# Kernel optimization log

Hardware: AMD Instinct MI355X
Metric: run time of the kernel (lower is better)

The kernel has to match this reference:

```python
import jax, jax.numpy as jnp
import numpy as np

D_MODEL = 512; D_INNER = 1024; D_STATE = 16; DT_RANK = 32; D_CONV = 4
N_LAYERS = 2; LSPP = 7; N_ROI = 2048; HIDDEN = 4096


def layer_norm(x, g, b, eps=1e-5):
    mu = x.mean(-1, keepdims=True)
    v = ((x - mu) ** 2).mean(-1, keepdims=True)
    return (x - mu) * jax.lax.rsqrt(v + eps) * g + b


def causal_dwconv(u, w, b):
    # u: [N,L,Di], w: [Di,K] depthwise, causal left-pad K-1
    x = jnp.transpose(u, (0, 2, 1))
    out = jax.lax.conv_general_dilated(x, w[:, None, :], (1,), [(D_CONV - 1, 0)],
                                       dimension_numbers=('NCH', 'OIH', 'NCH'),
                                       feature_group_count=D_INNER)
    return jnp.transpose(out, (0, 2, 1)) + b


def selective_scan(u, dt, A, B, C):
    # u, dt: [N,L,Di]; B, C: [N,L,S]; A: [Di,S]
    def step(h, xs):
        dt_t, B_t, C_t, u_t = xs
        dA = jnp.exp(dt_t[..., None] * A)                      # [N,Di,S]
        h = dA * h + (dt_t * u_t)[..., None] * B_t[:, None, :]
        return h, jnp.einsum('nds,ns->nd', h, C_t)
    h0 = jnp.zeros((u.shape[0], D_INNER, D_STATE), u.dtype)
    xs = (jnp.moveaxis(dt, 1, 0), jnp.moveaxis(B, 1, 0),
          jnp.moveaxis(C, 1, 0), jnp.moveaxis(u, 1, 0))
    _, ys = jax.lax.scan(step, h0, xs)
    return jnp.moveaxis(ys, 0, 1)                              # [N,L,Di]


def mamba_block(h, inw, cw, cb, xpw, dtw, dtb, Alog, Dp, ow):
    # decomposed bidirectional mamba ('dbm'): shared in_proj/gate, fwd+bwd scans summed
    xz = h @ inw.T                                             # [N,L,2*Di]
    xi, z = jnp.split(xz, 2, axis=-1)
    ys = []
    for d in range(2):
        u = xi if d == 0 else jnp.flip(xi, axis=1)
        u = jax.nn.silu(causal_dwconv(u, cw[d], cb[d]))
        dbl = u @ xpw[d].T                                     # [N,L,DT_RANK+2S]
        dtr = dbl[..., :DT_RANK]
        B = dbl[..., DT_RANK:DT_RANK + D_STATE]
        C = dbl[..., DT_RANK + D_STATE:]
        dt = jax.nn.softplus(dtr @ dtw[d].T + dtb[d])
        A = -jnp.exp(Alog[d])
        yd = selective_scan(u, dt, A, B, C) + u * Dp[d]
        ys.append(yd if d == 0 else jnp.flip(yd, axis=1))
    return ((ys[0] + ys[1]) * jax.nn.silu(z)) @ ow.T


def setup_inputs() -> dict:
    key = jax.random.key(0)
    ks = iter(jax.random.split(key, 40))
    rn = lambda shape, scale: jax.random.normal(next(ks), shape, dtype=jnp.float32) * scale
    inp = {}
    inp['x_flat'] = rn((N_ROI, D_MODEL * LSPP), 1.0)
    inp['conv_a_w'] = rn((256, 512, 3), (512 * 3) ** -0.5)
    inp['conv_p_w'] = rn((256, 512, 1), 512 ** -0.5)
    inp['se_w1'] = rn((32, 512), 512 ** -0.5)
    inp['se_b1'] = jnp.zeros((32,), jnp.float32)
    inp['se_w2'] = rn((512, 32), 32 ** -0.5)
    inp['se_b2'] = jnp.zeros((512,), jnp.float32)
    inp['ln_g'] = jnp.ones((N_LAYERS, D_MODEL), jnp.float32)
    inp['ln_b'] = jnp.zeros((N_LAYERS, D_MODEL), jnp.float32)
    inp['in_proj_w'] = rn((N_LAYERS, 2 * D_INNER, D_MODEL), D_MODEL ** -0.5)
    inp['conv_w'] = rn((N_LAYERS, 2, D_INNER, D_CONV), D_CONV ** -0.5)
    inp['conv_b'] = jnp.zeros((N_LAYERS, 2, D_INNER), jnp.float32)
    inp['x_proj_w'] = rn((N_LAYERS, 2, DT_RANK + 2 * D_STATE, D_INNER), D_INNER ** -0.5)
    inp['dt_proj_w'] = rn((N_LAYERS, 2, D_INNER, DT_RANK), DT_RANK ** -0.5)
    inp['dt_proj_b'] = rn((N_LAYERS, 2, D_INNER), 0.1) - 4.0
    inp['A_log'] = jnp.log(jnp.arange(1., D_STATE + 1., dtype=jnp.float32)) * jnp.ones((N_LAYERS, 2, D_INNER, D_STATE), jnp.float32)
    inp['D_param'] = jnp.ones((N_LAYERS, 2, D_INNER), jnp.float32)
    inp['out_proj_w'] = rn((N_LAYERS, D_MODEL, D_INNER), D_INNER ** -0.5)
    inp['out_ln_g'] = jnp.ones((D_MODEL,), jnp.float32)
    inp['out_ln_b'] = jnp.zeros((D_MODEL,), jnp.float32)
    inp['mlp_w1'] = rn((HIDDEN, D_MODEL), D_MODEL ** -0.5)
    inp['mlp_b1'] = jnp.zeros((HIDDEN,), jnp.float32)
    inp['mlp_w2'] = rn((HIDDEN, HIDDEN), HIDDEN ** -0.5)
    inp['mlp_b2'] = jnp.zeros((HIDDEN,), jnp.float32)
    return inp


def reference(x_flat, conv_a_w, conv_p_w, se_w1, se_b1, se_w2, se_b2, ln_g, ln_b,
              in_proj_w, conv_w, conv_b, x_proj_w, dt_proj_w, dt_proj_b, A_log,
              D_param, out_proj_w, out_ln_g, out_ln_b, mlp_w1, mlp_b1, mlp_w2, mlp_b2):
    N = x_flat.shape[0]
    x = x_flat.reshape(N, D_MODEL, LSPP)                       # [N,512,7]
    dn = ('NCH', 'OIH', 'NCH')
    # TSSE: strided conv branch + maxpool branch, concat, SE gating; L: 7 -> 4
    a = jax.nn.relu(jax.lax.conv_general_dilated(x, conv_a_w, (2,), [(1, 1)], dimension_numbers=dn))
    p = jax.lax.reduce_window(x, -jnp.inf, jax.lax.max, (1, 1, 3), (1, 1, 2), ((0, 0), (0, 0), (1, 1)))
    p = jax.nn.relu(jax.lax.conv_general_dilated(p, conv_p_w, (1,), [(0, 0)], dimension_numbers=dn))
    y = jnp.concatenate([a, p], axis=1)                        # [N,512,4]
    s = jax.nn.sigmoid(jax.nn.relu(y.mean(-1) @ se_w1.T + se_b1) @ se_w2.T + se_b2)
    y = y * s[:, :, None]
    # Mamba backbone: 2 pre-norm residual DBM blocks (mask is all-ones -> no-op)
    h = jnp.transpose(y, (0, 2, 1))                            # [N,L,512]
    for l in range(N_LAYERS):
        h = h + mamba_block(layer_norm(h, ln_g[l], ln_b[l]), in_proj_w[l], conv_w[l],
                            conv_b[l], x_proj_w[l], dt_proj_w[l], dt_proj_b[l],
                            A_log[l], D_param[l], out_proj_w[l])
    h = layer_norm(h, out_ln_g, out_ln_b)
    feat = h.mean(1)                                           # mean pool over time
    z1 = jax.nn.relu(feat @ mlp_w1.T + mlp_b1)
    return jax.nn.relu(z1 @ mlp_w2.T + mlp_b2)                 # [N,4096]
```

## Files before the change

kernel.cpp:

```cpp
#include <hip/hip_runtime.h>
#include <hip/hip_bf16.h>

typedef __hip_bfloat16 bf16;
typedef __attribute__((ext_vector_type(8))) short s16x8;
typedef __attribute__((ext_vector_type(4))) float f32x4;

__device__ __forceinline__ float u2f(unsigned short u){
  union { unsigned int i; float f; } v; v.i = ((unsigned int)u) << 16; return v.f;
}
__device__ __forceinline__ float bfu(bf16 x){ return __bfloat162float(x); }
__device__ __forceinline__ bf16  f2b(float x){ return __float2bfloat16(x); }

__device__ __forceinline__ void gload16(const void* g, void* l){
  __builtin_amdgcn_global_load_lds(
      (const __attribute__((address_space(1))) void*)g,
      (__attribute__((address_space(3))) void*)l, 16, 0, 0);
}

__device__ __forceinline__ float block_sum256(float v, float* red){
  #pragma unroll
  for (int o = 32; o > 0; o >>= 1) v += __shfl_down(v, o, 64);
  int lane = threadIdx.x & 63, wid = threadIdx.x >> 6;
  if (lane == 0) red[wid] = v;
  __syncthreads();
  float r = red[0] + red[1] + red[2] + red[3];
  __syncthreads();
  return r;
}

__global__ __launch_bounds__(256) void f2b4_kernel(
    const float4* __restrict__ in, ushort4* __restrict__ out, int n4)
{
  int stride = gridDim.x * 256;
  for (int i = blockIdx.x*256 + threadIdx.x; i < n4; i += stride){
    float4 v = in[i];
    ushort4 o;
    o.x = __bfloat16_as_ushort(f2b(v.x));
    o.y = __bfloat16_as_ushort(f2b(v.y));
    o.z = __bfloat16_as_ushort(f2b(v.z));
    o.w = __bfloat16_as_ushort(f2b(v.w));
    out[i] = o;
  }
}

__global__ __launch_bounds__(256) void xpw_pad_kernel(
    const float* __restrict__ xpw, bf16* __restrict__ out)
{
  int idx = blockIdx.x*256 + threadIdx.x;
  if (idx >= 524288) return;
  int l = idx >> 18, rem = idx & 262143, row = rem >> 10, c = rem & 1023;
  int d = row >> 7, r = row & 127;
  float v = (r < 64) ? xpw[(((size_t)l*2 + d)*64 + r)*1024 + c] : 0.f;
  out[idx] = f2b(v);
}

template<int ACT, int OMODE, bool HASBIAS>
__global__ __launch_bounds__(256) void mgemm_kernel(
    const bf16* __restrict__ A, const bf16* __restrict__ W,
    const float* __restrict__ bias, void* __restrict__ outp,
    int K, int ldo)
{
  __shared__ char lsA[16384];
  __shared__ char lsB[16384];
  const int tid = threadIdx.x;
  const int w = tid >> 6, l = tid & 63;
  const int nwg = gridDim.x * gridDim.y;
  const int lin = blockIdx.y * gridDim.x + blockIdx.x;
  const int cpx = nwg >> 3;
  const int swz = (lin & 7) * cpx + (lin >> 3);
  const int m0 = (swz % gridDim.x) * 128, n0 = (swz / gridDim.x) * 128;
  const int wr = w >> 1, wc = w & 1;
  const size_t ldb = (size_t)K * 2;
  const char* Ab = (const char*)A + (size_t)m0 * ldb;
  const char* Wb = (const char*)W + (size_t)n0 * ldb;

  const int srow = l >> 3;
  const int scb  = ((l & 7) ^ srow) << 4;

  const int fr = l & 15;
  const int fg = l >> 4;
  const int fsw = (fr & 7) << 4;

  f32x4 acc[4][4];
  #pragma unroll
  for (int m = 0; m < 4; ++m)
    #pragma unroll
    for (int n = 0; n < 4; ++n) acc[m][n] = (f32x4){0.f,0.f,0.f,0.f};

  const int nk = K >> 6;
  for (int kt = 0; kt < nk; ++kt){
    const char* As = Ab + (size_t)kt * 128;
    const char* Ws = Wb + (size_t)kt * 128;
    #pragma unroll
    for (int i = 0; i < 4; ++i){
      int row = (i*4 + w)*8 + srow;
      gload16(As + (size_t)row*ldb + scb, &lsA[(i*4 + w)*1024]);
    }
    #pragma unroll
    for (int i = 0; i < 4; ++i){
      int row = (i*4 + w)*8 + srow;
      gload16(Ws + (size_t)row*ldb + scb, &lsB[(i*4 + w)*1024]);
    }
    __syncthreads();

    s16x8 af[4][2], bfr[4][2];
    #pragma unroll
    for (int m = 0; m < 4; ++m){
      int row = wr*64 + m*16 + fr;
      af[m][0] = *(const s16x8*)&lsA[row*128 + (( 0 + fg*16) ^ fsw)];
      af[m][1] = *(const s16x8*)&lsA[row*128 + ((64 + fg*16) ^ fsw)];
    }
    #pragma unroll
    for (int n = 0; n < 4; ++n){
      int row = wc*64 + n*16 + fr;
      bfr[n][0] = *(const s16x8*)&lsB[row*128 + (( 0 + fg*16) ^ fsw)];
      bfr[n][1] = *(const s16x8*)&lsB[row*128 + ((64 + fg*16) ^ fsw)];
    }
    #pragma unroll
    for (int m = 0; m < 4; ++m)
      #pragma unroll
      for (int n = 0; n < 4; ++n){
        acc[m][n] = __builtin_amdgcn_mfma_f32_16x16x32_bf16(af[m][0], bfr[n][0], acc[m][n], 0, 0, 0);
        acc[m][n] = __builtin_amdgcn_mfma_f32_16x16x32_bf16(af[m][1], bfr[n][1], acc[m][n], 0, 0, 0);
      }
    __syncthreads();
  }

  const int orow0 = m0 + wr*64, ocol0 = n0 + wc*64;
  #pragma unroll
  for (int n = 0; n < 4; ++n){
    int col = ocol0 + n*16 + fr;
    float bv = HASBIAS ? bias[col] : 0.f;
    #pragma unroll
    for (int m = 0; m < 4; ++m){
      int rbase = orow0 + m*16 + fg*4;
      #pragma unroll
      for (int r = 0; r < 4; ++r){
        float v = acc[m][n][r] + bv;
        if (ACT == 1) v = fmaxf(v, 0.f);
        size_t oi = (size_t)(rbase + r) * ldo + col;
        if (OMODE == 0)      ((bf16*)outp)[oi] = f2b(v);
        else if (OMODE == 1) ((float*)outp)[oi] = v;
        else                 ((float*)outp)[oi] += v;
      }
    }
  }
}

__global__ __launch_bounds__(256) void bgemm_kernel(
    const bf16* __restrict__ A, const bf16* __restrict__ W,
    float* __restrict__ outp)
{
  __shared__ char lsA[16384];
  __shared__ char lsB[16384];
  const int tid = threadIdx.x;
  const int w = tid >> 6, l = tid & 63;
  const int nwg = gridDim.x * 2;
  const int lin = blockIdx.y * gridDim.x + blockIdx.x;
  const int cpx = nwg >> 3;
  const int swz = (lin & 7) * cpx + (lin >> 3);
  const int m0 = (swz % gridDim.x) * 128;
  const int d  = swz / gridDim.x;
  const int K = 1024, ldo = 256;
  const int wr = w >> 1, wc = w & 1;
  const size_t ldb = (size_t)K * 2;
  const char* Ab = (const char*)(A + (size_t)d*8388608) + (size_t)m0 * ldb;
  const char* Wb = (const char*)(W + (size_t)d*131072);

  const int srow = l >> 3;
  const int scb  = ((l & 7) ^ srow) << 4;
  const int fr = l & 15;
  const int fg = l >> 4;
  const int fsw = (fr & 7) << 4;

  f32x4 acc[4][4];
  #pragma unroll
  for (int m = 0; m < 4; ++m)
    #pragma unroll
    for (int n = 0; n < 4; ++n) acc[m][n] = (f32x4){0.f,0.f,0.f,0.f};

  const int nk = K >> 6;
  for (int kt = 0; kt < nk; ++kt){
    const char* As = Ab + (size_t)kt * 128;
    const char* Ws = Wb + (size_t)kt * 128;
    #pragma unroll
    for (int i = 0; i < 4; ++i){
      int row = (i*4 + w)*8 + srow;
      gload16(As + (size_t)row*ldb + scb, &lsA[(i*4 + w)*1024]);
    }
    #pragma unroll
    for (int i = 0; i < 4; ++i){
      int row = (i*4 + w)*8 + srow;
      gload16(Ws + (size_t)row*ldb + scb, &lsB[(i*4 + w)*1024]);
    }
    __syncthreads();

    s16x8 af[4][2], bfr[4][2];
    #pragma unroll
    for (int m = 0; m < 4; ++m){
      int row = wr*64 + m*16 + fr;
      af[m][0] = *(const s16x8*)&lsA[row*128 + (( 0 + fg*16) ^ fsw)];
      af[m][1] = *(const s16x8*)&lsA[row*128 + ((64 + fg*16) ^ fsw)];
    }
    #pragma unroll
    for (int n = 0; n < 4; ++n){
      int row = wc*64 + n*16 + fr;
      bfr[n][0] = *(const s16x8*)&lsB[row*128 + (( 0 + fg*16) ^ fsw)];
      bfr[n][1] = *(const s16x8*)&lsB[row*128 + ((64 + fg*16) ^ fsw)];
    }
    #pragma unroll
    for (int m = 0; m < 4; ++m)
      #pragma unroll
      for (int n = 0; n < 4; ++n){
        acc[m][n] = __builtin_amdgcn_mfma_f32_16x16x32_bf16(af[m][0], bfr[n][0], acc[m][n], 0, 0, 0);
        acc[m][n] = __builtin_amdgcn_mfma_f32_16x16x32_bf16(af[m][1], bfr[n][1], acc[m][n], 0, 0, 0);
      }
    __syncthreads();
  }

  const int orow0 = m0 + wr*64, ocol0 = d*128 + wc*64;
  #pragma unroll
  for (int n = 0; n < 4; ++n){
    int col = ocol0 + n*16 + fr;
    #pragma unroll
    for (int m = 0; m < 4; ++m){
      int rbase = orow0 + m*16 + fg*4;
      #pragma unroll
      for (int r = 0; r < 4; ++r)
        outp[(size_t)(rbase + r) * ldo + col] = acc[m][n][r];
    }
  }
}

__global__ __launch_bounds__(256) void im2col_kernel(
    const float* __restrict__ x_flat, bf16* __restrict__ Aa, bf16* __restrict__ P)
{
  __shared__ float xs[512][8];
  const int n = blockIdx.x, tid = threadIdx.x;
  const float* xr = x_flat + (size_t)n * 3584;
  for (int i = tid; i < 3584; i += 256) xs[i / 7][i % 7] = xr[i];
  __syncthreads();
  bf16* Ar = Aa + (size_t)n * 4 * 1536;
  for (int i = tid; i < 6144; i += 256){
    int t = i / 1536, col = i - t*1536;
    int c = col / 3, kk = col - c*3;
    int p = 2*t - 1 + kk;
    float v = (p >= 0 && p < 7) ? xs[c][p] : 0.f;
    Ar[i] = f2b(v);
  }
  bf16* Pr = P + (size_t)n * 4 * 512;
  for (int i = tid; i < 2048; i += 256){
    int t = i >> 9, c = i & 511;
    int st = 2*t - 1;
    float m = -1e30f;
    #pragma unroll
    for (int k = 0; k < 3; ++k){ int p = st + k; if (p >= 0 && p < 7) m = fmaxf(m, xs[c][p]); }
    Pr[i] = f2b(m);
  }
}

__global__ __launch_bounds__(256) void se_kernel(
    const float* __restrict__ sw1, const float* __restrict__ sb1,
    const float* __restrict__ sw2, const float* __restrict__ sb2,
    float* __restrict__ h)
{
  __shared__ float yms[512];
  __shared__ float s1s[32];
  const int n = blockIdx.x, tid = threadIdx.x;
  float* hb = h + (size_t)n * 2048;
  for (int c = tid; c < 512; c += 256)
    yms[c] = 0.25f * (hb[c] + hb[512+c] + hb[1024+c] + hb[1536+c]);
  __syncthreads();
  {
    int o = tid >> 3, sl = tid & 7;
    const float* wr = sw1 + (size_t)o * 512 + sl*64;
    const float* ym = yms + sl*64;
    float a = 0.f;
    #pragma unroll 16
    for (int i = 0; i < 64; ++i) a += wr[i] * ym[i];
    a += __shfl_down(a, 4, 8);
    a += __shfl_down(a, 2, 8);
    a += __shfl_down(a, 1, 8);
    if (sl == 0) s1s[o] = fmaxf(a + sb1[o], 0.f);
  }
  __syncthreads();
  for (int c = tid; c < 512; c += 256){
    float a = sb2[c];
    const float* wr = sw2 + (size_t)c * 32;
    #pragma unroll
    for (int j = 0; j < 32; ++j) a += wr[j] * s1s[j];
    float s = 1.f / (1.f + __expf(-a));
    #pragma unroll
    for (int t = 0; t < 4; ++t) hb[t*512 + c] *= s;
  }
}

__global__ __launch_bounds__(256) void ln_kernel(
    const float* __restrict__ x, const float* __restrict__ g,
    const float* __restrict__ b, bf16* __restrict__ out)
{
  __shared__ float red[4];
  const int row = blockIdx.x, t = threadIdx.x;
  const float* xr = x + (size_t)row * 512;
  float v0 = xr[t], v1 = xr[t + 256];
  float s = block_sum256(v0 + v1, red);
  float mu = s * (1.f/512.f);
  float d0 = v0 - mu, d1 = v1 - mu;
  float sq = block_sum256(d0*d0 + d1*d1, red);
  float rstd = rsqrtf(sq * (1.f/512.f) + 1e-5f);
  out[(size_t)row*512 + t]       = f2b(d0*rstd*g[t]     + b[t]);
  out[(size_t)row*512 + t + 256] = f2b(d1*rstd*g[t+256] + b[t+256]);
}

__global__ __launch_bounds__(256) void finalln_kernel(
    const float* __restrict__ h, const float* __restrict__ g,
    const float* __restrict__ b, bf16* __restrict__ feat)
{
  __shared__ float red[4];
  const int n = blockIdx.x, t = threadIdx.x;
  float a0 = 0.f, a1 = 0.f;
  for (int tt = 0; tt < 4; ++tt){
    const float* xr = h + ((size_t)n*4 + tt)*512;
    float v0 = xr[t], v1 = xr[t+256];
    float s = block_sum256(v0 + v1, red);
    float mu = s * (1.f/512.f);
    float d0 = v0 - mu, d1 = v1 - mu;
    float sq = block_sum256(d0*d0 + d1*d1, red);
    float rstd = rsqrtf(sq * (1.f/512.f) + 1e-5f);
    a0 += d0*rstd*g[t]     + b[t];
    a1 += d1*rstd*g[t+256] + b[t+256];
  }
  feat[(size_t)n*512 + t]       = f2b(a0 * 0.25f);
  feat[(size_t)n*512 + t + 256] = f2b(a1 * 0.25f);
}

__global__ __launch_bounds__(256) void dwconv2_kernel(
    const bf16* __restrict__ xz, const float* __restrict__ cw,
    const float* __restrict__ cb, bf16* __restrict__ u)
{
  const int n = blockIdx.x;
  const int c4 = threadIdx.x * 4;
  ushort4 in4[4];
  #pragma unroll
  for (int t = 0; t < 4; ++t)
    in4[t] = *reinterpret_cast<const ushort4*>(&xz[((size_t)n*4 + t)*2048 + c4]);
  #pragma unroll
  for (int d = 0; d < 2; ++d){
    const float* cwd = cw + d*4096;
    const float* cbd = cb + d*1024;
    ushort4 out[4];
    #pragma unroll
    for (int j = 0; j < 4; ++j){
      float xa[4];
      #pragma unroll
      for (int t = 0; t < 4; ++t){
        int ts = d ? 3 - t : t;
        unsigned short us = j==0?in4[ts].x : j==1?in4[ts].y : j==2?in4[ts].z : in4[ts].w;
        xa[t] = u2f(us);
      }
      float4 wv = *reinterpret_cast<const float4*>(&cwd[(c4 + j)*4]);
      float bb = cbd[c4 + j];
      float o[4];
      o[0] = xa[0]*wv.w + bb;
      o[1] = xa[0]*wv.z + xa[1]*wv.w + bb;
      o[2] = xa[0]*wv.y + xa[1]*wv.z + xa[2]*wv.w + bb;
      o[3] = xa[0]*wv.x + xa[1]*wv.y + xa[2]*wv.z + xa[3]*wv.w + bb;
      #pragma unroll
      for (int t = 0; t < 4; ++t){
        float v = o[t];
        float sv = v / (1.f + __expf(-v));
        unsigned short us = __bfloat16_as_ushort(f2b(sv));
        if (j==0) out[t].x = us; else if (j==1) out[t].y = us;
        else if (j==2) out[t].z = us; else out[t].w = us;
      }
    }
    #pragma unroll
    for (int t = 0; t < 4; ++t)
      *reinterpret_cast<ushort4*>(&u[(size_t)d*8388608 + ((size_t)n*4 + t)*1024 + c4]) = out[t];
  }
}

__global__ __launch_bounds__(256) void scan_kernel(
    const float* __restrict__ dbl, const float* __restrict__ dtw,
    const float* __restrict__ dtb, const bf16* __restrict__ u,
    const float* __restrict__ Alog, const float* __restrict__ Dp,
    bf16* __restrict__ y)
{
  __shared__ float dtr[4][32];
  __shared__ float Bs[4][16], Cs[4][16];
  const int n = blockIdx.x, g = blockIdx.y, d = blockIdx.z, tid = threadIdx.x;
  {
    int t = tid >> 6, j = tid & 63;
    float v = dbl[((size_t)n*4 + t)*256 + d*128 + j];
    if (j < 32) dtr[t][j] = v;
    else if (j < 48) Bs[t][j-32] = v;
    else Cs[t][j-48] = v;
  }
  __syncthreads();
  const int c = g*256 + tid;
  float wdt[32];
  {
    const float4* wp4 = reinterpret_cast<const float4*>(dtw + (size_t)d*32768 + (size_t)c*32);
    #pragma unroll
    for (int q = 0; q < 8; ++q){
      float4 v = wp4[q];
      wdt[q*4+0] = v.x; wdt[q*4+1] = v.y; wdt[q*4+2] = v.z; wdt[q*4+3] = v.w;
    }
  }
  const float dtbc = dtb[d*1024 + c];
  const float* Ald = Alog + (size_t)d*16384;
  float A[16];
  #pragma unroll
  for (int s = 0; s < 16; ++s) A[s] = -__expf(Ald[(size_t)c*16 + s]);
  const float Dpc = Dp[d*1024 + c];
  const bf16* ud = u + (size_t)d*8388608;
  bf16* yd = y + (size_t)d*8388608;
  float hs[16];
  #pragma unroll
  for (int s = 0; s < 16; ++s) hs[s] = 0.f;
  #pragma unroll
  for (int t = 0; t < 4; ++t){
    float raw = dtbc;
    #pragma unroll
    for (int k = 0; k < 32; ++k) raw += dtr[t][k] * wdt[k];
    float dtv = (raw > 20.f) ? raw : log1pf(__expf(raw));
    float uv  = bfu(ud[((size_t)n*4 + t)*1024 + c]);
    float du = dtv * uv;
    float yv = 0.f;
    #pragma unroll
    for (int s = 0; s < 16; ++s){
      float dA = __expf(dtv * A[s]);
      hs[s] = dA * hs[s] + du * Bs[t][s];
      yv += hs[s] * Cs[t][s];
    }
    float out = yv + uv * Dpc;
    int to = d ? (3 - t) : t;
    yd[((size_t)n*4 + to)*1024 + c] = f2b(out);
  }
}

__global__ __launch_bounds__(256) void gate_kernel(
    const bf16* __restrict__ y, const bf16* __restrict__ xz,
    bf16* __restrict__ gated)
{
  const int total4 = 8192 * 256;
  for (int i = blockIdx.x*256 + threadIdx.x; i < total4; i += 2048*256){
    int row = i >> 8, c4 = (i & 255) << 2;
    ushort4 a4 = reinterpret_cast<const ushort4*>(y)[i];
    ushort4 b4 = reinterpret_cast<const ushort4*>(y + 8388608)[i];
    ushort4 z4 = *reinterpret_cast<const ushort4*>(&xz[(size_t)row*2048 + 1024 + c4]);
    float y0 = u2f(a4.x) + u2f(b4.x), y1 = u2f(a4.y) + u2f(b4.y);
    float y2 = u2f(a4.z) + u2f(b4.z), y3 = u2f(a4.w) + u2f(b4.w);
    float z0 = u2f(z4.x), z1 = u2f(z4.y), z2 = u2f(z4.z), z3 = u2f(z4.w);
    ushort4 o;
    o.x = __bfloat16_as_ushort(f2b(y0 * z0 / (1.f + __expf(-z0))));
    o.y = __bfloat16_as_ushort(f2b(y1 * z1 / (1.f + __expf(-z1))));
    o.z = __bfloat16_as_ushort(f2b(y2 * z2 / (1.f + __expf(-z2))));
    o.w = __bfloat16_as_ushort(f2b(y3 * z3 / (1.f + __expf(-z3))));
    reinterpret_cast<ushort4*>(gated)[i] = o;
  }
}

extern "C" void kernel_launch(void* const* d_in, const int* in_sizes, int n_in,
                              void* d_out, int out_size, void* d_ws, size_t ws_size,
                              hipStream_t stream)
{
  const float* x_flat    = (const float*)d_in[0];
  const float* conv_a_w  = (const float*)d_in[1];
  const float* conv_p_w  = (const float*)d_in[2];
  const float* se_w1     = (const float*)d_in[3];
  const float* se_b1     = (const float*)d_in[4];
  const float* se_w2     = (const float*)d_in[5];
  const float* se_b2     = (const float*)d_in[6];
  const float* ln_g      = (const float*)d_in[7];
  const float* ln_b      = (const float*)d_in[8];
  const float* in_proj_w = (const float*)d_in[9];
  const float* conv_w    = (const float*)d_in[10];
  const float* conv_b    = (const float*)d_in[11];
  const float* x_proj_w  = (const float*)d_in[12];
  const float* dt_proj_w = (const float*)d_in[13];
  const float* dt_proj_b = (const float*)d_in[14];
  const float* A_log     = (const float*)d_in[15];
  const float* D_param   = (const float*)d_in[16];
  const float* out_proj_w= (const float*)d_in[17];
  const float* out_ln_g  = (const float*)d_in[18];
  const float* out_ln_b  = (const float*)d_in[19];
  const float* mlp_w1    = (const float*)d_in[20];
  const float* mlp_b1    = (const float*)d_in[21];
  const float* mlp_w2    = (const float*)d_in[22];
  const float* mlp_b2    = (const float*)d_in[23];

  char* ws = (char*)d_ws;
  const size_t OFF_H    = 0;
  const size_t OFF_HN   = OFF_H    + 16777216;
  const size_t OFF_XZ   = OFF_HN   + 8388608;
  const size_t OFF_U    = OFF_XZ   + 33554432;
  const size_t OFF_SCR  = OFF_U    + 33554432;
  const size_t OFF_YB   = OFF_SCR  + 25165824;
  const size_t OFF_WB   = OFF_YB   + 33554432;
  const size_t OFF_WXP  = OFF_WB   + 6291456;

  float* h    = (float*)(ws + OFF_H);
  bf16*  hn   = (bf16*) (ws + OFF_HN);
  bf16*  xz   = (bf16*) (ws + OFF_XZ);
  bf16*  u    = (bf16*) (ws + OFF_U);
  float* dbl  = (float*)(ws + OFF_SCR);
  bf16*  y    = (bf16*) (ws + OFF_YB);
  bf16*  feat = (bf16*) (ws + OFF_HN);
  bf16*  z1   = (bf16*) (ws + OFF_XZ);
  bf16*  wbi  = (bf16*) (ws + OFF_WB);
  bf16*  wbo  = (bf16*) (ws + OFF_WB + 4194304);
  bf16*  wxp  = (bf16*) (ws + OFF_WXP);
  bf16*  wb1  = (bf16*) (ws + OFF_SCR);
  bf16*  wb2  = (bf16*) (ws + OFF_YB);
  bf16*  Aa   = (bf16*) (ws + OFF_SCR);
  bf16*  Pm   = (bf16*) (ws + OFF_YB);
  bf16*  wa   = (bf16*) (ws + OFF_YB + 8388608);
  bf16*  wp   = (bf16*) (ws + OFF_YB + 8388608 + 786432);
  float* outf = (float*)d_out;

  f2b4_kernel<<<512,  256, 0, stream>>>((const float4*)conv_a_w,   (ushort4*)wa,  98304);
  f2b4_kernel<<<256,  256, 0, stream>>>((const float4*)conv_p_w,   (ushort4*)wp,  32768);
  f2b4_kernel<<<2048, 256, 0, stream>>>((const float4*)in_proj_w,  (ushort4*)wbi, 524288);
  f2b4_kernel<<<1024, 256, 0, stream>>>((const float4*)out_proj_w, (ushort4*)wbo, 262144);
  xpw_pad_kernel<<<2048, 256, 0, stream>>>(x_proj_w, wxp);

  im2col_kernel<<<2048, 256, 0, stream>>>(x_flat, Aa, Pm);
  mgemm_kernel<1,1,false><<<dim3(64,2), 256, 0, stream>>>(
      Aa, wa, nullptr, h, 1536, 512);
  mgemm_kernel<1,1,false><<<dim3(64,2), 256, 0, stream>>>(
      Pm, wp, nullptr, (float*)h + 256, 512, 512);
  se_kernel<<<2048, 256, 0, stream>>>(se_w1, se_b1, se_w2, se_b2, h);

  for (int l = 0; l < 2; ++l){
    ln_kernel<<<8192, 256, 0, stream>>>(h, ln_g + l*512, ln_b + l*512, hn);
    mgemm_kernel<0,0,false><<<dim3(64,16), 256, 0, stream>>>(
        hn, wbi + (size_t)l*2048*512, nullptr, xz, 512, 2048);
    dwconv2_kernel<<<2048, 256, 0, stream>>>(
        xz, conv_w + (size_t)l*8192, conv_b + (size_t)l*2048, u);
    bgemm_kernel<<<dim3(64,2), 256, 0, stream>>>(
        u, wxp + (size_t)l*262144, dbl);
    scan_kernel<<<dim3(2048,4,2), 256, 0, stream>>>(
        dbl, dt_proj_w + (size_t)l*65536, dt_proj_b + (size_t)l*2048,
        u, A_log + (size_t)l*32768, D_param + (size_t)l*2048, y);
    gate_kernel<<<2048, 256, 0, stream>>>(y, xz, u );
    mgemm_kernel<0,2,false><<<dim3(64,4), 256, 0, stream>>>(
        u, wbo + (size_t)l*512*1024, nullptr, h, 1024, 512);
  }

  finalln_kernel<<<2048, 256, 0, stream>>>(h, out_ln_g, out_ln_b, feat);

  f2b4_kernel<<<1024, 256, 0, stream>>>((const float4*)mlp_w1, (ushort4*)wb1, 524288);
  f2b4_kernel<<<2048, 256, 0, stream>>>((const float4*)mlp_w2, (ushort4*)wb2, 4194304);

  mgemm_kernel<1,0,true><<<dim3(16,32), 256, 0, stream>>>(
      feat, wb1, mlp_b1, z1, 512, 4096);
  mgemm_kernel<1,1,true><<<dim3(16,32), 256, 0, stream>>>(
      z1, wb2, mlp_b2, outf, 4096, 4096);
}
```

Before: 750.4 us.

## Move dt projection out of scan into MFMA GEMM with fused softplus

The per-thread 32-term dt_proj dot product inside the scan kernel is replaced by a separate bf16 MFMA GEMM per direction (K padded to 64) with softplus fused into its epilogue. The x_proj GEMM now writes dt-rank as bf16 and B/C as a compact fp32 buffer. A = -exp(A_log) is precomputed once into a table. The aim is to cut the scan kernel's ALU work and weight loads. In exchange it adds extra launches, a bf16 round-trip for dt (a precision loss), and splits the scan into two launches per layer.

Result: no change. 738.5 us (-1.6%).

```diff
diff --git a/kernel.cpp b/kernel.cpp
--- a/kernel.cpp
+++ b/kernel.cpp
@@ -52,6 +52,23 @@
   int d = row >> 7, r = row & 127;
   float v = (r < 64) ? xpw[(((size_t)l*2 + d)*64 + r)*1024 + c] : 0.f;
   out[idx] = f2b(v);
+}
+
+__global__ __launch_bounds__(256) void wdt_pad_kernel(
+    const float* __restrict__ dtw, bf16* __restrict__ out)
+{
+  int idx = blockIdx.x*256 + threadIdx.x;
+  if (idx >= 262144) return;
+  int ld = idx >> 16, rem = idx & 65535, r = rem >> 6, c = rem & 63;
+  float v = (c < 32) ? dtw[((size_t)ld*1024 + r)*32 + c] : 0.f;
+  out[idx] = f2b(v);
+}
+
+__global__ __launch_bounds__(256) void atab_kernel(
+    const float* __restrict__ Alog, float* __restrict__ Atab)
+{
+  int i = blockIdx.x*256 + threadIdx.x;
+  if (i < 65536) Atab[i] = -__expf(Alog[i]);
 }
 
 template<int ACT, int OMODE, bool HASBIAS>
@@ -76,7 +93,6 @@
 
   const int srow = l >> 3;
   const int scb  = ((l & 7) ^ srow) << 4;
-
   const int fr = l & 15;
   const int fg = l >> 4;
   const int fsw = (fr & 7) << 4;
@@ -138,6 +154,7 @@
       for (int r = 0; r < 4; ++r){
         float v = acc[m][n][r] + bv;
         if (ACT == 1) v = fmaxf(v, 0.f);
+        if (ACT == 2) v = (v > 20.f) ? v : log1pf(__expf(v));
         size_t oi = (size_t)(rbase + r) * ldo + col;
         if (OMODE == 0)      ((bf16*)outp)[oi] = f2b(v);
         else if (OMODE == 1) ((float*)outp)[oi] = v;
@@ -149,7 +166,7 @@
 
 __global__ __launch_bounds__(256) void bgemm_kernel(
     const bf16* __restrict__ A, const bf16* __restrict__ W,
-    float* __restrict__ outp)
+    bf16* __restrict__ dtr_buf, float* __restrict__ dbl)
 {
   __shared__ char lsA[16384];
   __shared__ char lsB[16384];
@@ -161,7 +178,7 @@
   const int swz = (lin & 7) * cpx + (lin >> 3);
   const int m0 = (swz % gridDim.x) * 128;
   const int d  = swz / gridDim.x;
-  const int K = 1024, ldo = 256;
+  const int K = 1024;
   const int wr = w >> 1, wc = w & 1;
   const size_t ldb = (size_t)K * 2;
   const char* Ab = (const char*)(A + (size_t)d*8388608) + (size_t)m0 * ldb;
@@ -218,16 +235,24 @@
     __syncthreads();
   }
 
-  const int orow0 = m0 + wr*64, ocol0 = d*128 + wc*64;
+  const int orow0 = m0 + wr*64, c0 = wc*64;
   #pragma unroll
   for (int n = 0; n < 4; ++n){
-    int col = ocol0 + n*16 + fr;
+    int col = c0 + n*16 + fr;
     #pragma unroll
     for (int m = 0; m < 4; ++m){
       int rbase = orow0 + m*16 + fg*4;
       #pragma unroll
-      for (int r = 0; r < 4; ++r)
-        outp[(size_t)(rbase + r) * ldo + col] = acc[m][n][r];
+      for (int r = 0; r < 4; ++r){
+        float v = acc[m][n][r];
+        int row = rbase + r;
+        if (col < 32)
+          dtr_buf[((size_t)d*8192 + row)*64 + col] = f2b(v);
+        else if (col < 64)
+          dbl[(size_t)row*128 + d*64 + (col - 32)] = v;
+        else if (col < 96)
+          dtr_buf[((size_t)d*8192 + row)*64 + (col - 32)] = f2b(v);
+      }
     }
   }
 }
@@ -381,49 +406,35 @@
 }
 
 __global__ __launch_bounds__(256) void scan_kernel(
-    const float* __restrict__ dbl, const float* __restrict__ dtw,
-    const float* __restrict__ dtb, const bf16* __restrict__ u,
-    const float* __restrict__ Alog, const float* __restrict__ Dp,
-    bf16* __restrict__ y)
-{
-  __shared__ float dtr[4][32];
+    const float* __restrict__ dbl, const bf16* __restrict__ dt,
+    const bf16* __restrict__ ud, const float* __restrict__ Atab,
+    const float* __restrict__ Dp, int d, bf16* __restrict__ yd)
+{
   __shared__ float Bs[4][16], Cs[4][16];
-  const int n = blockIdx.x, g = blockIdx.y, d = blockIdx.z, tid = threadIdx.x;
-  {
-    int t = tid >> 6, j = tid & 63;
-    float v = dbl[((size_t)n*4 + t)*256 + d*128 + j];
-    if (j < 32) dtr[t][j] = v;
-    else if (j < 48) Bs[t][j-32] = v;
-    else Cs[t][j-48] = v;
+  const int n = blockIdx.x, g = blockIdx.y, tid = threadIdx.x;
+  if (tid < 128){
+    int t = tid >> 5, j = tid & 31;
+    float v = dbl[((size_t)n*4 + t)*128 + d*64 + j];
+    if (j < 16) Bs[t][j] = v; else Cs[t][j-16] = v;
   }
   __syncthreads();
   const int c = g*256 + tid;
-  float wdt[32];
+  float A[16];
   {
-    const float4* wp4 = reinterpret_cast<const float4*>(dtw + (size_t)d*32768 + (size_t)c*32);
-    #pragma unroll
-    for (int q = 0; q < 8; ++q){
-      float4 v = wp4[q];
-      wdt[q*4+0] = v.x; wdt[q*4+1] = v.y; wdt[q*4+2] = v.z; wdt[q*4+3] = v.w;
-    }
-  }
-  const float dtbc = dtb[d*1024 + c];
-  const float* Ald = Alog + (size_t)d*16384;
-  float A[16];
-  #pragma unroll
-  for (int s = 0; s < 16; ++s) A[s] = -__expf(Ald[(size_t)c*16 + s]);
-  const float Dpc = Dp[d*1024 + c];
-  const bf16* ud = u + (size_t)d*8388608;
-  bf16* yd = y + (size_t)d*8388608;
+    const float4* ap = reinterpret_cast<const float4*>(Atab + (size_t)c*16);
+    #pragma unroll
+    for (int q = 0; q < 4; ++q){
+      float4 v = ap[q];
+      A[q*4+0] = v.x; A[q*4+1] = v.y; A[q*4+2] = v.z; A[q*4+3] = v.w;
+    }
+  }
+  const float Dpc = Dp[c];
   float hs[16];
   #pragma unroll
   for (int s = 0; s < 16; ++s) hs[s] = 0.f;
   #pragma unroll
   for (int t = 0; t < 4; ++t){
-    float raw = dtbc;
-    #pragma unroll
-    for (int k = 0; k < 32; ++k) raw += dtr[t][k] * wdt[k];
-    float dtv = (raw > 20.f) ? raw : log1pf(__expf(raw));
+    float dtv = bfu(dt[((size_t)n*4 + t)*1024 + c]);
     float uv  = bfu(ud[((size_t)n*4 + t)*1024 + c]);
     float du = dtv * uv;
     float yv = 0.f;
@@ -499,18 +510,24 @@
   const size_t OFF_YB   = OFF_SCR  + 25165824;
   const size_t OFF_WB   = OFF_YB   + 33554432;
   const size_t OFF_WXP  = OFF_WB   + 6291456;
+  const size_t OFF_WDT  = OFF_WXP  + 1048576;
+  const size_t OFF_ATAB = OFF_WDT  + 524288;
 
   float* h    = (float*)(ws + OFF_H);
   bf16*  hn   = (bf16*) (ws + OFF_HN);
   bf16*  xz   = (bf16*) (ws + OFF_XZ);
   bf16*  u    = (bf16*) (ws + OFF_U);
   float* dbl  = (float*)(ws + OFF_SCR);
+  bf16*  dtrb = (bf16*) (ws + OFF_SCR + 4194304);
+  bf16*  dtb_ = (bf16*) (ws + OFF_SCR + 6291456);
   bf16*  y    = (bf16*) (ws + OFF_YB);
   bf16*  feat = (bf16*) (ws + OFF_HN);
   bf16*  z1   = (bf16*) (ws + OFF_XZ);
   bf16*  wbi  = (bf16*) (ws + OFF_WB);
   bf16*  wbo  = (bf16*) (ws + OFF_WB + 4194304);
   bf16*  wxp  = (bf16*) (ws + OFF_WXP);
+  bf16*  wdtp = (bf16*) (ws + OFF_WDT);
+  float* Atab = (float*)(ws + OFF_ATAB);
   bf16*  wb1  = (bf16*) (ws + OFF_SCR);
   bf16*  wb2  = (bf16*) (ws + OFF_YB);
   bf16*  Aa   = (bf16*) (ws + OFF_SCR);
@@ -524,6 +541,8 @@
   f2b4_kernel<<<2048, 256, 0, stream>>>((const float4*)in_proj_w,  (ushort4*)wbi, 524288);
   f2b4_kernel<<<1024, 256, 0, stream>>>((const float4*)out_proj_w, (ushort4*)wbo, 262144);
   xpw_pad_kernel<<<2048, 256, 0, stream>>>(x_proj_w, wxp);
+  wdt_pad_kernel<<<1024, 256, 0, stream>>>(dt_proj_w, wdtp);
+  atab_kernel<<<256, 256, 0, stream>>>(A_log, Atab);
 
   im2col_kernel<<<2048, 256, 0, stream>>>(x_flat, Aa, Pm);
   mgemm_kernel<1,1,false><<<dim3(64,2), 256, 0, stream>>>(
@@ -539,10 +558,16 @@
     dwconv2_kernel<<<2048, 256, 0, stream>>>(
         xz, conv_w + (size_t)l*8192, conv_b + (size_t)l*2048, u);
     bgemm_kernel<<<dim3(64,2), 256, 0, stream>>>(
-        u, wxp + (size_t)l*262144, dbl);
-    scan_kernel<<<dim3(2048,4,2), 256, 0, stream>>>(
-        dbl, dt_proj_w + (size_t)l*65536, dt_proj_b + (size_t)l*2048,
-        u, A_log + (size_t)l*32768, D_param + (size_t)l*2048, y);
+        u, wxp + (size_t)l*262144, dtrb, dbl);
+    for (int d = 0; d < 2; ++d){
+      int ld = l*2 + d;
+      mgemm_kernel<2,0,true><<<dim3(64,8), 256, 0, stream>>>(
+          dtrb + (size_t)d*8192*64, wdtp + (size_t)ld*65536,
+          dt_proj_b + (size_t)ld*1024, dtb_, 64, 1024);
+      scan_kernel<<<dim3(2048,4), 256, 0, stream>>>(
+          dbl, dtb_, u + (size_t)d*8388608, Atab + (size_t)ld*16384,
+          D_param + (size_t)ld*1024, d, y + (size_t)d*8388608);
+    }
     gate_kernel<<<2048, 256, 0, stream>>>(y, xz, u );
     mgemm_kernel<0,2,false><<<dim3(64,4), 256, 0, stream>>>(
         u, wbo + (size_t)l*512*1024, nullptr, h, 1024, 512);
```
